# Kernel optimization log

Hardware: AMD Instinct MI355X
Metric: run time of the kernel (lower is better)

## Reference

```python
import jax, jax.numpy as jnp
import numpy as np

B, T, E, H = 4096, 256, 27, 64


def setup_inputs() -> dict:
    key = jax.random.key(0)
    k1, k2, k3, k4, k5 = jax.random.split(key, 5)
    word = jax.random.uniform(k1, (B, T, E), dtype=jnp.float32)
    # Kaiming-ish scaling for linear layers
    Wa = jax.random.normal(k2, (H, H + E), dtype=jnp.float32) / np.sqrt(H + E)
    ba = jax.random.normal(k3, (H,), dtype=jnp.float32) * 0.01
    Wy = jax.random.normal(k4, (E, H), dtype=jnp.float32) / np.sqrt(H)
    by = jax.random.normal(k5, (E,), dtype=jnp.float32) * 0.01
    return {"word": word, "Wa": Wa, "ba": ba, "Wy": Wy, "by": by}


def reference(word, Wa, ba, Wy, by):
    batch, Tx, emb = word.shape
    hidden = Wa.shape[0]
    # Split concat-linear into two matmuls: concat((a,x)) @ Wa.T == a @ Waa.T + x @ Wax.T
    Waa = Wa[:, :hidden]   # [H, H]
    Wax = Wa[:, hidden:]   # [H, E]

    word_t = jnp.transpose(word, (1, 0, 2))  # [Tx, batch, E]

    def step(carry, w_t):
        a, x = carry
        next_a = jnp.tanh(a @ Waa.T + x @ Wax.T + ba)  # [batch, H]
        hat_y = next_a @ Wy.T + by                      # [batch, E]
        return (next_a, w_t), hat_y

    a0 = jnp.zeros((batch, hidden), dtype=word.dtype)
    x0 = jnp.zeros((batch, emb), dtype=word.dtype)
    _, ys = jax.lax.scan(step, (a0, x0), word_t)  # ys: [Tx, batch, E]
    return jnp.transpose(ys, (1, 0, 2))           # [batch, Tx, E]
```

## Files before the change

### kernel.cpp

```cpp
#include <hip/hip_runtime.h>
#include <stdint.h>


#define B_ 4096
#define T_ 256
#define E_ 27
#define H_ 64
#define WROW_ (H_ + E_)

typedef _Float16 f16x8 __attribute__((ext_vector_type(8)));
typedef float f32x4 __attribute__((ext_vector_type(4)));
typedef unsigned int u32x4 __attribute__((ext_vector_type(4)));
typedef unsigned int u32x2 __attribute__((ext_vector_type(2)));

struct __attribute__((packed)) f4a { float v[4]; };

static __device__ __forceinline__ unsigned pkf16(float a, float b) {
  _Float16 ha = (_Float16)a, hb = (_Float16)b;
  unsigned short ua = __builtin_bit_cast(unsigned short, ha);
  unsigned short ub = __builtin_bit_cast(unsigned short, hb);
  return (unsigned)ua | ((unsigned)ub << 16);
}
static __device__ __forceinline__ unsigned pkrtz(float a, float b) {
  unsigned r;
  asm("v_cvt_pkrtz_f16_f32 %0, %1, %2" : "=v"(r) : "v"(a), "v"(b));
  return r;
}
static __device__ __forceinline__ float fast_tanh(float z) {
  float e = __expf(2.0f * z);
  float r = __builtin_amdgcn_rcpf(e + 1.0f);
  return __builtin_fmaf(-2.0f, r, 1.0f);
}
static __device__ __forceinline__ f32x4 MFH(u32x4 a, u32x4 b, f32x4 c) {
  return __builtin_amdgcn_mfma_f32_16x16x32_f16(
      __builtin_bit_cast(f16x8, a), __builtin_bit_cast(f16x8, b), c, 0, 0, 0);
}

__global__ __launch_bounds__(256)
__attribute__((amdgpu_waves_per_eu(1, 1))) void rnn_fused(
    const float* __restrict__ word, const float* __restrict__ Wa,
    const float* __restrict__ ba, const float* __restrict__ Wy,
    const float* __restrict__ by, float* __restrict__ out) {
  __shared__ __align__(16) float xs[8][16][36];
  __shared__ __align__(16) float ys[16][16][36];
  __shared__ __align__(16) unsigned int sxc[2][4][16][12];

  const int tid = threadIdx.x;
  const int wv = tid >> 6;
  const int lane = tid & 63;
  const int p16 = lane & 15;
  const int lg = lane >> 4;
  const int rb = (int)blockIdx.x * 16;

  const float* const wbase = word + (size_t)(rb + p16) * (T_ * E_);
  float* const obase = out + (size_t)(rb + p16) * (T_ * E_);

  for (int i = tid; i < 8 * 16 * 36; i += 256) (&xs[0][0][0])[i] = 0.f;

  u32x4 WH0, WH1, WXw, WY0, WY1;
  f32x4 BAv, BYv;
  {
    const float* base = Wa + (16 * wv + p16) * WROW_;
#pragma unroll
    for (int v = 0; v < 4; ++v) {
      const int j = 2 * v;
      const int c0 = (j < 4) ? (4 * lg + j) : (12 + 4 * lg + j);
      WH0[v] = pkf16(base[c0], base[c0 + 1]);
      WH1[v] = pkf16(base[c0 + 32], base[c0 + 33]);
      const int e0 = 8 * lg + j, e1 = e0 + 1;
      const float w0 = (e0 < E_) ? base[H_ + e0] : 0.f;
      const float w1 = (e1 < E_) ? base[H_ + e1] : 0.f;
      WXw[v] = pkf16(w0, w1);
    }
  }
  {
    const int e = 16 * (wv & 1) + p16;
    const bool valid = (e < E_);
    const float* rp = Wy + e * H_;
#pragma unroll
    for (int v = 0; v < 4; ++v) {
      const int j = 2 * v;
      const int c0 = (j < 4) ? (4 * lg + j) : (12 + 4 * lg + j);
      WY0[v] = pkf16(valid ? rp[c0] : 0.f, valid ? rp[c0 + 1] : 0.f);
      WY1[v] = pkf16(valid ? rp[c0 + 32] : 0.f, valid ? rp[c0 + 33] : 0.f);
    }
  }
#pragma unroll
  for (int r = 0; r < 4; ++r) BAv[r] = ba[16 * wv + 4 * lg + r];
#pragma unroll
  for (int r = 0; r < 4; ++r) {
    const int e = 16 * (wv & 1) + 4 * lg + r;
    BYv[r] = (e < E_) ? by[e] : 0.f;
  }

  f32x4 Rg[2][7];
#define X_ISSUE(ts, P)                                                      \
  {                                                                         \
    const int st_ = (ts) + lg;                                              \
    if (st_ >= 1 && st_ < T_) {                                             \
      const float* p_ = wbase + (st_ - 1) * E_;                             \
      _Pragma("unroll") for (int c = 0; c < 7; ++c) {                       \
        asm volatile("global_load_dwordx4 %0, %1, off"                      \
                     : "=v"(Rg[P][c]) : "v"(p_ + 4 * c) : "memory");        \
      }                                                                     \
    }                                                                       \
  }
#define X_WRITE(ts, P)                                                      \
  {                                                                         \
    asm volatile("s_waitcnt vmcnt(0)" ::: "memory");                        \
    __builtin_amdgcn_sched_barrier(0);                                      \
    const int st_ = (ts) + lg;                                              \
    if (st_ >= 1 && st_ < T_) {                                             \
      float* d_ = &xs[st_ & 7][p16][0];                                     \
      _Pragma("unroll") for (int c = 0; c < 7; ++c)                         \
        *(f32x4*)(d_ + 4 * c) = Rg[P][c];                                   \
    }                                                                       \
    asm volatile("s_waitcnt lgkmcnt(0)" ::: "memory");                      \
    __builtin_amdgcn_sched_barrier(0);                                      \
  }
#define Y_FLUSH(tb)                                                         \
  {                                                                         \
    const float* s_ = &ys[((tb) + lg) & 15][p16][0];                        \
    float* d_ = obase + (size_t)((tb) + lg) * E_;                           \
    _Pragma("unroll") for (int c = 0; c < 6; ++c) {                         \
      f32x4 v_ = *(const f32x4*)(s_ + 4 * c);                               \
      f4a o_;                                                               \
      o_.v[0] = v_[0]; o_.v[1] = v_[1]; o_.v[2] = v_[2]; o_.v[3] = v_[3];   \
      *(f4a*)(d_ + 4 * c) = o_;                                             \
    }                                                                       \
    f32x4 v6_ = *(const f32x4*)(s_ + 24);                                   \
    d_[24] = v6_[0]; d_[25] = v6_[1]; d_[26] = v6_[2];                      \
  }

  if (wv == 0) X_ISSUE(0, 0);
  __syncthreads();
  if (wv == 0) { X_WRITE(0, 0); X_ISSUE(4, 1); }
  __syncthreads();
  f32x4 xc0, xc1;
  {
    const float* xp = &xs[1][p16][8 * lg];
    xc0 = *(const f32x4*)xp;
    xc1 = *(const f32x4*)(xp + 4);
  }

  u32x4 sF0 = {0u, 0u, 0u, 0u}, sF1 = sF0;
  f32x4 zp = BAv;

#define STEP(t)                                                               \
  {                                                                           \
                \
    f32x4 d_ = MFH(WH0, sF0, zp);                                             \
    d_ = MFH(WH1, sF1, d_);                                                   \
             \
    if (wv < 2) {                                                             \
      f32x4 yv = MFH(WY1, sF1, MFH(WY0, sF0, BYv));                           \
      *(f32x4*)&ys[((t) + 15) & 15][p16][(wv & 1) * 16 + 4 * lg] = yv;        \
    }                                                                         \
                  \
    u32x4 xfn;                                                                \
    xfn[0] = pkrtz(xc0[0], xc0[1]);                                           \
    xfn[1] = pkrtz(xc0[2], xc0[3]);                                           \
    xfn[2] = pkrtz(xc1[0], xc1[1]);                                           \
    xfn[3] = pkrtz(xc1[2], xc1[3]);                                           \
    zp = MFH(WXw, xfn, BAv);                                                  \
    if ((t) + 2 < T_) {                                                       \
      const float* xp_ = &xs[((t) + 2) & 7][p16][8 * lg];                     \
      xc0 = *(const f32x4*)xp_;                                               \
      xc1 = *(const f32x4*)(xp_ + 4);                                         \
    }                                                                         \
            \
    const float t0_ = fast_tanh(d_[0]);                                       \
    const float t1_ = fast_tanh(d_[1]);                                       \
    const float t2_ = fast_tanh(d_[2]);                                       \
    const float t3_ = fast_tanh(d_[3]);                                       \
    u32x2 pk_;                                                                \
    pk_[0] = pkf16(t0_, t1_);                                                 \
    pk_[1] = pkf16(t2_, t3_);                                                 \
    *(u32x2*)&sxc[(t) & 1][lg][p16][2 * wv] = pk_;                            \
    asm volatile("s_waitcnt lgkmcnt(0)" ::: "memory");                        \
    __builtin_amdgcn_sched_barrier(0);                                        \
    __builtin_amdgcn_s_barrier();                                             \
    __builtin_amdgcn_sched_barrier(0);                                        \
                          \
    sF0 = *(const u32x4*)&sxc[(t) & 1][lg][p16][0];                           \
    sF1 = *(const u32x4*)&sxc[(t) & 1][lg][p16][4];                           \
  }

#define GROUP(t0, PW, PI)                                                     \
  {                                                                           \
    asm volatile("" : "+a"(WH0), "+a"(WH1), "+a"(WXw), "+a"(WY0), "+a"(WY1)); \
    asm volatile("" : "+v"(BAv), "+v"(BYv));                                  \
    if (wv == 0) { X_WRITE((t0) + 4, PW); X_ISSUE((t0) + 8, PI); }            \
    if (wv == 2 && (t0) >= 8) Y_FLUSH((t0)-8);                                \
    STEP(t0);                                                                 \
    STEP((t0) + 1);                                                           \
    STEP((t0) + 2);                                                           \
    STEP((t0) + 3);                                                           \
  }

  for (int t0 = 0; t0 < T_; t0 += 8) {
    GROUP(t0, 1, 0);
    GROUP(t0 + 4, 0, 1);
  }
  if (wv < 2) {
    f32x4 yv = MFH(WY1, sF1, MFH(WY0, sF0, BYv));
    *(f32x4*)&ys[15][p16][(wv & 1) * 16 + 4 * lg] = yv;
  }
  asm volatile("s_waitcnt lgkmcnt(0)" ::: "memory");
  __builtin_amdgcn_s_barrier();
  if (wv == 2) {
    Y_FLUSH(T_ - 8);
    Y_FLUSH(T_ - 4);
  }
#undef GROUP
#undef STEP
#undef X_ISSUE
#undef X_WRITE
#undef Y_FLUSH
}

extern "C" void kernel_launch(void* const* d_in, const int* in_sizes, int n_in,
                              void* d_out, int out_size, void* d_ws,
                              size_t ws_size, hipStream_t stream) {
  const float* word = (const float*)d_in[0];
  const float* Wa = (const float*)d_in[1];
  const float* ba = (const float*)d_in[2];
  const float* Wy = (const float*)d_in[3];
  const float* by = (const float*)d_in[4];
  float* out = (float*)d_out;
  rnn_fused<<<dim3(B_ / 16), dim3(256), 0, stream>>>(word, Wa, ba, Wy, by, out);
}
```

Baseline: 87.40 us.

## Spread x loads and y stores across all waves and split the recurrent MFMA chain

The global loads of word, the LDS staging of x and the output flushes, previously done only by wave 0 or wave 2, are now split across all four waves, each handling one timestep. The shared hidden-state buffer is relaid out as [buf][wave][lg][p16][2] so that the hidden fragments are read at the start of each step rather than after the barrier. The two dependent hidden MFMAs become two independent MFMAs whose results are summed, which shortens the critical path per step. This spreads load and store issue more evenly across waves and shortens the serial recurrence, at the cost of an extra vector add and more scattered LDS reads.

```diff
diff --git a/kernel.cpp b/kernel.cpp
--- a/kernel.cpp
+++ b/kernel.cpp
@@ -43,7 +43,7 @@
     const float* __restrict__ by, float* __restrict__ out) {
   __shared__ __align__(16) float xs[8][16][36];
   __shared__ __align__(16) float ys[16][16][36];
-  __shared__ __align__(16) unsigned int sxc[2][4][16][12];
+  __shared__ __align__(8) unsigned int sxc[2][4][4][16][2];
 
   const int tid = threadIdx.x;
   const int wv = tid >> 6;
@@ -56,6 +56,8 @@
   float* const obase = out + (size_t)(rb + p16) * (T_ * E_);
 
   for (int i = tid; i < 8 * 16 * 36; i += 256) (&xs[0][0][0])[i] = 0.f;
+  for (int i = tid; i < 2 * 4 * 4 * 16 * 2; i += 256)
+    (&sxc[0][0][0][0][0])[i] = 0u;
 
   u32x4 WH0, WH1, WXw, WY0, WY1;
   f32x4 BAv, BYv;
@@ -93,48 +95,56 @@
     BYv[r] = (e < E_) ? by[e] : 0.f;
   }
 
-  f32x4 Rg[2][7];
+  f32x4 Rg[2][2];
 #define X_ISSUE(ts, P)                                                      \
   {                                                                         \
-    const int st_ = (ts) + lg;                                              \
+    const int st_ = (ts) + wv;                                              \
     if (st_ >= 1 && st_ < T_) {                                             \
       const float* p_ = wbase + (st_ - 1) * E_;                             \
-      _Pragma("unroll") for (int c = 0; c < 7; ++c) {                       \
+      asm volatile("global_load_dwordx4 %0, %1, off"                        \
+                   : "=v"(Rg[P][0]) : "v"(p_ + 8 * lg) : "memory");         \
+      if (lg < 3)                                                           \
         asm volatile("global_load_dwordx4 %0, %1, off"                      \
-                     : "=v"(Rg[P][c]) : "v"(p_ + 4 * c) : "memory");        \
-      }                                                                     \
+                     : "=v"(Rg[P][1]) : "v"(p_ + 8 * lg + 4) : "memory");   \
     }                                                                       \
   }
 #define X_WRITE(ts, P)                                                      \
   {                                                                         \
     asm volatile("s_waitcnt vmcnt(0)" ::: "memory");                        \
     __builtin_amdgcn_sched_barrier(0);                                      \
-    const int st_ = (ts) + lg;                                              \
+    const int st_ = (ts) + wv;                                              \
     if (st_ >= 1 && st_ < T_) {                                             \
       float* d_ = &xs[st_ & 7][p16][0];                                     \
-      _Pragma("unroll") for (int c = 0; c < 7; ++c)                         \
-        *(f32x4*)(d_ + 4 * c) = Rg[P][c];                                   \
+      *(f32x4*)(d_ + 8 * lg) = Rg[P][0];                                    \
+      if (lg < 3) *(f32x4*)(d_ + 8 * lg + 4) = Rg[P][1];                    \
     }                                                                       \
     asm volatile("s_waitcnt lgkmcnt(0)" ::: "memory");                      \
     __builtin_amdgcn_sched_barrier(0);                                      \
   }
 #define Y_FLUSH(tb)                                                         \
   {                                                                         \
-    const float* s_ = &ys[((tb) + lg) & 15][p16][0];                        \
-    float* d_ = obase + (size_t)((tb) + lg) * E_;                           \
-    _Pragma("unroll") for (int c = 0; c < 6; ++c) {                         \
-      f32x4 v_ = *(const f32x4*)(s_ + 4 * c);                               \
-      f4a o_;                                                               \
-      o_.v[0] = v_[0]; o_.v[1] = v_[1]; o_.v[2] = v_[2]; o_.v[3] = v_[3];   \
-      *(f4a*)(d_ + 4 * c) = o_;                                             \
+    const int s_t = (tb) + wv;                                              \
+    const float* s_ = &ys[s_t & 15][p16][0];                                \
+    float* d_ = obase + (size_t)s_t * E_;                                   \
+    if (lg < 3) {                                                           \
+      f32x4 v0_ = *(const f32x4*)(s_ + 8 * lg);                             \
+      f32x4 v1_ = *(const f32x4*)(s_ + 8 * lg + 4);                         \
+      f4a o0_, o1_;                                                         \
+      o0_.v[0] = v0_[0]; o0_.v[1] = v0_[1];                                 \
+      o0_.v[2] = v0_[2]; o0_.v[3] = v0_[3];                                 \
+      o1_.v[0] = v1_[0]; o1_.v[1] = v1_[1];                                 \
+      o1_.v[2] = v1_[2]; o1_.v[3] = v1_[3];                                 \
+      *(f4a*)(d_ + 8 * lg) = o0_;                                           \
+      *(f4a*)(d_ + 8 * lg + 4) = o1_;                                       \
+    } else {                                                                \
+      d_[24] = s_[24]; d_[25] = s_[25]; d_[26] = s_[26];                    \
     }                                                                       \
-    f32x4 v6_ = *(const f32x4*)(s_ + 24);                                   \
-    d_[24] = v6_[0]; d_[25] = v6_[1]; d_[26] = v6_[2];                      \
-  }
-
-  if (wv == 0) X_ISSUE(0, 0);
+  }
+
+  X_ISSUE(0, 0);
   __syncthreads();
-  if (wv == 0) { X_WRITE(0, 0); X_ISSUE(4, 1); }
+  X_WRITE(0, 0);
+  X_ISSUE(4, 1);
   __syncthreads();
   f32x4 xc0, xc1;
   {
@@ -143,32 +153,41 @@
     xc1 = *(const f32x4*)(xp + 4);
   }
 
-  u32x4 sF0 = {0u, 0u, 0u, 0u}, sF1 = sF0;
   f32x4 zp = BAv;
+  const f32x4 zf4 = {0.f, 0.f, 0.f, 0.f};
 
 #define STEP(t)                                                               \
   {                                                                           \
-                \
-    f32x4 d_ = MFH(WH0, sF0, zp);                                             \
-    d_ = MFH(WH1, sF1, d_);                                                   \
-             \
-    if (wv < 2) {                                                             \
-      f32x4 yv = MFH(WY1, sF1, MFH(WY0, sF0, BYv));                           \
-      *(f32x4*)&ys[((t) + 15) & 15][p16][(wv & 1) * 16 + 4 * lg] = yv;        \
-    }                                                                         \
-                  \
+           \
+    const u32x2 r0_ = *(const u32x2*)&sxc[((t) + 1) & 1][0][lg][p16][0];      \
+    const u32x2 r1_ = *(const u32x2*)&sxc[((t) + 1) & 1][1][lg][p16][0];      \
+    const u32x2 r2_ = *(const u32x2*)&sxc[((t) + 1) & 1][2][lg][p16][0];      \
+    const u32x2 r3_ = *(const u32x2*)&sxc[((t) + 1) & 1][3][lg][p16][0];      \
+        \
     u32x4 xfn;                                                                \
     xfn[0] = pkrtz(xc0[0], xc0[1]);                                           \
     xfn[1] = pkrtz(xc0[2], xc0[3]);                                           \
     xfn[2] = pkrtz(xc1[0], xc1[1]);                                           \
     xfn[3] = pkrtz(xc1[2], xc1[3]);                                           \
-    zp = MFH(WXw, xfn, BAv);                                                  \
+    const f32x4 zpn_ = MFH(WXw, xfn, BAv);                                    \
     if ((t) + 2 < T_) {                                                       \
       const float* xp_ = &xs[((t) + 2) & 7][p16][8 * lg];                     \
       xc0 = *(const f32x4*)xp_;                                               \
       xc1 = *(const f32x4*)(xp_ + 4);                                         \
     }                                                                         \
-            \
+                  \
+    u32x4 sF0_, sF1_;                                                         \
+    sF0_[0] = r0_[0]; sF0_[1] = r0_[1]; sF0_[2] = r1_[0]; sF0_[3] = r1_[1];   \
+    sF1_[0] = r2_[0]; sF1_[1] = r2_[1]; sF1_[2] = r3_[0]; sF1_[3] = r3_[1];   \
+             \
+    const f32x4 pa_ = MFH(WH0, sF0_, zp);                                     \
+    const f32x4 pb_ = MFH(WH1, sF1_, zf4);                                    \
+    if (wv < 2) {                                                             \
+      const f32x4 yv_ = MFH(WY1, sF1_, MFH(WY0, sF0_, BYv));                  \
+      *(f32x4*)&ys[((t) + 15) & 15][p16][(wv & 1) * 16 + 4 * lg] = yv_;       \
+    }                                                                         \
+    const f32x4 d_ = pa_ + pb_;                                               \
+                       \
     const float t0_ = fast_tanh(d_[0]);                                       \
     const float t1_ = fast_tanh(d_[1]);                                       \
     const float t2_ = fast_tanh(d_[2]);                                       \
@@ -176,22 +195,21 @@
     u32x2 pk_;                                                                \
     pk_[0] = pkf16(t0_, t1_);                                                 \
     pk_[1] = pkf16(t2_, t3_);                                                 \
-    *(u32x2*)&sxc[(t) & 1][lg][p16][2 * wv] = pk_;                            \
+    *(u32x2*)&sxc[(t) & 1][wv][lg][p16][0] = pk_;                             \
+    zp = zpn_;                                                                \
     asm volatile("s_waitcnt lgkmcnt(0)" ::: "memory");                        \
     __builtin_amdgcn_sched_barrier(0);                                        \
     __builtin_amdgcn_s_barrier();                                             \
     __builtin_amdgcn_sched_barrier(0);                                        \
-                          \
-    sF0 = *(const u32x4*)&sxc[(t) & 1][lg][p16][0];                           \
-    sF1 = *(const u32x4*)&sxc[(t) & 1][lg][p16][4];                           \
   }
 
 #define GROUP(t0, PW, PI)                                                     \
   {                                                                           \
     asm volatile("" : "+a"(WH0), "+a"(WH1), "+a"(WXw), "+a"(WY0), "+a"(WY1)); \
     asm volatile("" : "+v"(BAv), "+v"(BYv));                                  \
-    if (wv == 0) { X_WRITE((t0) + 4, PW); X_ISSUE((t0) + 8, PI); }            \
-    if (wv == 2 && (t0) >= 8) Y_FLUSH((t0)-8);                                \
+    X_WRITE((t0) + 4, PW);    \
+    X_ISSUE((t0) + 8, PI);        \
+    if ((t0) >= 8) Y_FLUSH((t0)-8);               \
     STEP(t0);                                                                 \
     STEP((t0) + 1);                                                           \
     STEP((t0) + 2);                                                           \
@@ -203,15 +221,20 @@
     GROUP(t0 + 4, 0, 1);
   }
   if (wv < 2) {
-    f32x4 yv = MFH(WY1, sF1, MFH(WY0, sF0, BYv));
-    *(f32x4*)&ys[15][p16][(wv & 1) * 16 + 4 * lg] = yv;
+    const u32x2 r0_ = *(const u32x2*)&sxc[1][0][lg][p16][0];
+    const u32x2 r1_ = *(const u32x2*)&sxc[1][1][lg][p16][0];
+    const u32x2 r2_ = *(const u32x2*)&sxc[1][2][lg][p16][0];
+    const u32x2 r3_ = *(const u32x2*)&sxc[1][3][lg][p16][0];
+    u32x4 sF0_, sF1_;
+    sF0_[0] = r0_[0]; sF0_[1] = r0_[1]; sF0_[2] = r1_[0]; sF0_[3] = r1_[1];
+    sF1_[0] = r2_[0]; sF1_[1] = r2_[1]; sF1_[2] = r3_[0]; sF1_[3] = r3_[1];
+    const f32x4 yv_ = MFH(WY1, sF1_, MFH(WY0, sF0_, BYv));
+    *(f32x4*)&ys[15][p16][(wv & 1) * 16 + 4 * lg] = yv_;
   }
   asm volatile("s_waitcnt lgkmcnt(0)" ::: "memory");
   __builtin_amdgcn_s_barrier();
-  if (wv == 2) {
-    Y_FLUSH(T_ - 8);
-    Y_FLUSH(T_ - 4);
-  }
+  Y_FLUSH(T_ - 8);
+  Y_FLUSH(T_ - 4);
 #undef GROUP
 #undef STEP
 #undef X_ISSUE
```

Result: slower. 99.83 us (+14.2%).
